# Performance work log

Measured on AMD Instinct MI355X. Metric: run time of the kernel, lower is better.

## Reference

```python
import jax, jax.numpy as jnp
import numpy as np

HEADS = 8
DIM_HEAD = 64
BOTTLENECK = 40


def setup_inputs() -> dict:
    key = jax.random.key(0)
    ks = jax.random.split(key, 10)
    b, n, qs = 4, 1024, 256
    inner = HEADS * DIM_HEAD
    s = lambda fan_in: 1.0 / np.sqrt(fan_in)
    return {
        "x":   jax.random.normal(ks[0], (b, n, qs), dtype=jnp.float32),
        # weights stored as (in, out) so forward is x @ W
        "wq1": jax.random.normal(ks[1], (qs, BOTTLENECK), dtype=jnp.float32) * s(qs),
        "wq2": jax.random.normal(ks[2], (BOTTLENECK, inner), dtype=jnp.float32) * s(BOTTLENECK),
        "wk1": jax.random.normal(ks[3], (qs, BOTTLENECK), dtype=jnp.float32) * s(qs),
        "wk2": jax.random.normal(ks[4], (BOTTLENECK, inner), dtype=jnp.float32) * s(BOTTLENECK),
        "wv1": jax.random.normal(ks[5], (qs, BOTTLENECK), dtype=jnp.float32) * s(qs),
        "wv2": jax.random.normal(ks[6], (BOTTLENECK, inner), dtype=jnp.float32) * s(BOTTLENECK),
        "wo":  jax.random.normal(ks[7], (inner, qs), dtype=jnp.float32) * s(inner),
        "bo":  jax.random.normal(ks[8], (qs,), dtype=jnp.float32) * 0.01,
    }


def reference(x, wq1, wq2, wk1, wk2, wv1, wv2, wo, bo):
    b, n, _ = x.shape
    h, d = HEADS, DIM_HEAD
    scale = d ** -0.5

    # bottlenecked QKV projections (40-dim), SiLU on K bottleneck
    q = (x @ wq1) @ wq2                       # (b, n, h*d)
    k = jax.nn.silu(x @ wk1) @ wk2            # (b, n, h*d)
    v = (x @ wv1) @ wv2                       # (b, n, h*d)

    def split(t):  # 'b n (h d) -> b (h n) d'
        return t.reshape(b, n, h, d).transpose(0, 2, 1, 3).reshape(b, h * n, d)

    q, k, v = split(q), split(k), split(v)

    sim = jnp.einsum('bid,bjd->bij', q, k) * scale   # (b, h*n, h*n)
    attn = jax.nn.softmax(sim, axis=-1)
    out = jnp.einsum('bij,bjd->bid', attn, v)        # (b, h*n, d)

    # 'b (h n) d -> b n (h d)'
    out = out.reshape(b, h, n, d).transpose(0, 2, 1, 3).reshape(b, n, h * d)
    return out @ wo + bo
```

## Files before the change

### kernel.cpp

```cpp
#include <hip/hip_runtime.h>
#include <hip/hip_bf16.h>


#define B_    4
#define H_    8
#define NSEQ  1024
#define SEQ   8192
#define DH    64
#define QS    256
#define INNER 512
#define QSCALE 0.18033688011112042f

#define KVSW_BATCH 524288

typedef __bf16 bf16x8 __attribute__((ext_vector_type(8)));
typedef float floatx4 __attribute__((ext_vector_type(4)));

__global__ __launch_bounds__(1024) void qkv_kernel(
    const float* __restrict__ x,
    const float* __restrict__ wq1, const float* __restrict__ wq2,
    const float* __restrict__ wk1, const float* __restrict__ wk2,
    const float* __restrict__ wv1, const float* __restrict__ wv2,
    __hip_bfloat16* __restrict__ Qg, __hip_bfloat16* __restrict__ KSg,
    __hip_bfloat16* __restrict__ VSg)
{
  const int tid  = threadIdx.x;
  const int b    = blockIdx.x >> 6;
  const int nblk = blockIdx.x & 63;
  const int n0   = nblk << 4;

  __shared__ __align__(16) float xs[16][260];
  __shared__ __align__(16) float tb2[2][3][16][40];
  __shared__ __align__(16) float tb[3][16][40];
  __shared__ __align__(16) __hip_bfloat16 qb[16][520];
  __shared__ __align__(16) __hip_bfloat16 kb[16][520];
  __shared__ __align__(16) __hip_bfloat16 vb[512][20];

  for (int i = tid; i < 16 * 256; i += 1024) {
    const int r = i >> 8, c = i & 255;
    xs[r][c] = x[((size_t)b * NSEQ + n0 + r) * QS + c];
  }
  __syncthreads();

  if (tid < 960) {
    const int ks  = (tid >= 480) ? 1 : 0;
    const int t2  = tid - ks * 480;
    const int p   = t2 / 160;
    const int rem = t2 - p * 160;
    const int r   = rem / 10;
    const int bn  = (rem - r * 10) * 4;
    const float* w1 = (p == 0) ? wq1 : (p == 1) ? wk1 : wv1;
    float a0 = 0.f, a1 = 0.f, a2 = 0.f, a3 = 0.f;
    #pragma unroll 4
    for (int c4 = ks * 32; c4 < ks * 32 + 32; ++c4) {
      const float4 xv = *(const float4*)(&xs[r][c4 * 4]);
      const float4 wa = *(const float4*)(w1 + (c4 * 4 + 0) * 40 + bn);
      const float4 wb = *(const float4*)(w1 + (c4 * 4 + 1) * 40 + bn);
      const float4 wc = *(const float4*)(w1 + (c4 * 4 + 2) * 40 + bn);
      const float4 wd = *(const float4*)(w1 + (c4 * 4 + 3) * 40 + bn);
      a0 += xv.x * wa.x + xv.y * wb.x + xv.z * wc.x + xv.w * wd.x;
      a1 += xv.x * wa.y + xv.y * wb.y + xv.z * wc.y + xv.w * wd.y;
      a2 += xv.x * wa.z + xv.y * wb.z + xv.z * wc.z + xv.w * wd.z;
      a3 += xv.x * wa.w + xv.y * wb.w + xv.z * wc.w + xv.w * wd.w;
    }
    tb2[ks][p][r][bn + 0] = a0; tb2[ks][p][r][bn + 1] = a1;
    tb2[ks][p][r][bn + 2] = a2; tb2[ks][p][r][bn + 3] = a3;
  }
  __syncthreads();

  if (tid < 480) {
    const int p   = tid / 160;
    const int rem = tid - p * 160;
    const int r   = rem / 10;
    const int bn  = (rem - r * 10) * 4;
    const float4 h0 = *(const float4*)(&tb2[0][p][r][bn]);
    const float4 h1 = *(const float4*)(&tb2[1][p][r][bn]);
    float a0 = h0.x + h1.x, a1 = h0.y + h1.y, a2 = h0.z + h1.z, a3 = h0.w + h1.w;
    if (p == 1) {
      a0 = a0 / (1.f + __expf(-a0));
      a1 = a1 / (1.f + __expf(-a1));
      a2 = a2 / (1.f + __expf(-a2));
      a3 = a3 / (1.f + __expf(-a3));
    }
    tb[p][r][bn + 0] = a0; tb[p][r][bn + 1] = a1;
    tb[p][r][bn + 2] = a2; tb[p][r][bn + 3] = a3;
  }
  __syncthreads();

  #pragma unroll
  for (int pass = 0; pass < 3; ++pass) {
    const int p  = pass;
    const int cq = tid & 127;
    const int rq = (tid >> 7) & 7;
    const int c  = cq * 4, r0 = rq * 2;
    const float* w2 = (p == 0) ? wq2 : (p == 1) ? wk2 : wv2;
    const float scale = (p == 0) ? QSCALE : 1.0f;
    float acc[2][4];
    #pragma unroll
    for (int i = 0; i < 2; ++i)
      #pragma unroll
      for (int j = 0; j < 4; ++j) acc[i][j] = 0.f;

    #pragma unroll 2
    for (int jb = 0; jb < 10; ++jb) {
      const float4 w0 = *(const float4*)(w2 + (jb * 4 + 0) * INNER + c);
      const float4 w1r = *(const float4*)(w2 + (jb * 4 + 1) * INNER + c);
      const float4 w2r = *(const float4*)(w2 + (jb * 4 + 2) * INNER + c);
      const float4 w3 = *(const float4*)(w2 + (jb * 4 + 3) * INNER + c);
      #pragma unroll
      for (int ri = 0; ri < 2; ++ri) {
        const float4 tv = *(const float4*)(&tb[p][r0 + ri][jb * 4]);
        acc[ri][0] += tv.x * w0.x + tv.y * w1r.x + tv.z * w2r.x + tv.w * w3.x;
        acc[ri][1] += tv.x * w0.y + tv.y * w1r.y + tv.z * w2r.y + tv.w * w3.y;
        acc[ri][2] += tv.x * w0.z + tv.y * w1r.z + tv.z * w2r.z + tv.w * w3.z;
        acc[ri][3] += tv.x * w0.w + tv.y * w1r.w + tv.z * w2r.w + tv.w * w3.w;
      }
    }
    #pragma unroll
    for (int ri = 0; ri < 2; ++ri)
      #pragma unroll
      for (int ci = 0; ci < 4; ++ci) {
        const int cc = c + ci;
        const float v = acc[ri][ci] * scale;
        if (p == 0)      qb[r0 + ri][cc] = __float2bfloat16(v);
        else if (p == 1) kb[r0 + ri][cc] = __float2bfloat16(v);
        else             vb[cc][r0 + ri] = __float2bfloat16(v);
      }
  }
  __syncthreads();

  {
    const int i  = tid;
    const int h  = i >> 7;
    const int r  = (i >> 3) & 15;
    const int d8 = i & 7;
    *(float4*)(Qg + ((size_t)b * SEQ + h * NSEQ + n0 + r) * DH + d8 * 8) =
        *(const float4*)(&qb[r][h * 64 + d8 * 8]);
  }

  {
    const int i    = tid;
    const int h    = i >> 7;
    const int ks   = (i >> 6) & 1;
    const int quad = (i >> 4) & 3;
    const int r    = i & 15;
    const int lane = quad * 16 + r;
    const size_t dst = (size_t)b * KVSW_BATCH
        + ((size_t)((h * 64 + nblk) * 2 + ks) * 64 + lane) * 8;
    *(float4*)(KSg + dst) = *(const float4*)(&kb[r][h * 64 + ks * 32 + quad * 8]);
  }

  {
    const int st  = nblk & 1;
    const int p32 = nblk >> 1;
    #pragma unroll
    for (int pass = 0; pass < 2; ++pass) {
      const int i   = tid + pass * 1024;
      const int h   = i >> 8;
      const int dnt = (i >> 6) & 3;
      const int dm  = (i >> 2) & 15;
      const int rg  = i & 3;
      const int lane = rg * 16 + dm;
      const size_t dst = (size_t)b * KVSW_BATCH
          + ((size_t)((h * 32 + p32) * 4 + dnt) * 64 + lane) * 8 + st * 4;
      *(uint2*)(VSg + dst) = *(const uint2*)(&vb[h * 64 + dnt * 16 + dm][rg * 4]);
    }
  }
}

struct PairBuf {
  bf16x8 k[2][2];
  bf16x8 v[4];
};

__global__ __launch_bounds__(256, 3) void attn_kernel(
    const __hip_bfloat16* __restrict__ Qg,
    const __hip_bfloat16* __restrict__ KSg,
    const __hip_bfloat16* __restrict__ VSg,
    float* __restrict__ OPg,
    float* __restrict__ PSg)
{
  __shared__ float Osh[4][16][68];
  __shared__ float psums[4][64];

  const int tid  = threadIdx.x;
  const int wave = tid >> 6;
  const int lane = tid & 63;
  const int lrow = lane & 15;
  const int quad = lane >> 4;

  const int xcd   = blockIdx.x & 7;
  const int idx   = blockIdx.x >> 3;
  const int b     = xcd >> 1;
  const int half  = idx & 1;
  const int qtile = (xcd & 1) * 64 + (idx >> 1);
  const int qbase = qtile * 64;

  const __hip_bfloat16* Qb  = Qg + ((size_t)b * SEQ + qbase) * DH;
  const __hip_bfloat16* kp0 = KSg + (size_t)b * KVSW_BATCH + half * 262144
                              + (size_t)wave * 65536 + lane * 8;
  const __hip_bfloat16* vp0 = VSg + (size_t)b * KVSW_BATCH + half * 262144
                              + (size_t)wave * 65536 + lane * 8;

  bf16x8 qf[4][2];
  #pragma unroll
  for (int mt = 0; mt < 4; ++mt)
    #pragma unroll
    for (int s = 0; s < 2; ++s)
      qf[mt][s] = *(const bf16x8*)(Qb + (mt * 16 + lrow) * DH + s * 32 + quad * 8);

  floatx4 oacc[4][4];
  #pragma unroll
  for (int mt = 0; mt < 4; ++mt)
    #pragma unroll
    for (int dnt = 0; dnt < 4; ++dnt)
      oacc[mt][dnt] = (floatx4){0.f, 0.f, 0.f, 0.f};
  float psum[4] = {0.f, 0.f, 0.f, 0.f};

  #pragma unroll 2
  for (int pair = 0; pair < 32; ++pair) {
    PairBuf pb;
    const __hip_bfloat16* kp = kp0 + pair * 2048;
    pb.k[0][0] = *(const bf16x8*)(kp);
    pb.k[0][1] = *(const bf16x8*)(kp + 512);
    pb.k[1][0] = *(const bf16x8*)(kp + 1024);
    pb.k[1][1] = *(const bf16x8*)(kp + 1536);
    const __hip_bfloat16* vp = vp0 + pair * 2048;
    #pragma unroll
    for (int dnt = 0; dnt < 4; ++dnt)
      pb.v[dnt] = *(const bf16x8*)(vp + dnt * 512);

    #pragma unroll
    for (int mt = 0; mt < 4; ++mt) {
      floatx4 s0 = (floatx4){0.f, 0.f, 0.f, 0.f};
      floatx4 s1 = (floatx4){0.f, 0.f, 0.f, 0.f};
      s0 = __builtin_amdgcn_mfma_f32_16x16x32_bf16(pb.k[0][0], qf[mt][0], s0, 0, 0, 0);
      s0 = __builtin_amdgcn_mfma_f32_16x16x32_bf16(pb.k[0][1], qf[mt][1], s0, 0, 0, 0);
      s1 = __builtin_amdgcn_mfma_f32_16x16x32_bf16(pb.k[1][0], qf[mt][0], s1, 0, 0, 0);
      s1 = __builtin_amdgcn_mfma_f32_16x16x32_bf16(pb.k[1][1], qf[mt][1], s1, 0, 0, 0);
      float p[8];
      #pragma unroll
      for (int r = 0; r < 4; ++r) {
        p[r]     = __builtin_amdgcn_exp2f(s0[r]);
        p[4 + r] = __builtin_amdgcn_exp2f(s1[r]);
      }
      psum[mt] += ((p[0] + p[1]) + (p[2] + p[3])) + ((p[4] + p[5]) + (p[6] + p[7]));
      bf16x8 pa;
      #pragma unroll
      for (int j = 0; j < 8; ++j) pa[j] = (__bf16)p[j];
      #pragma unroll
      for (int dnt = 0; dnt < 4; ++dnt)
        oacc[mt][dnt] = __builtin_amdgcn_mfma_f32_16x16x32_bf16(pa, pb.v[dnt], oacc[mt][dnt], 0, 0, 0);
    }
  }

  #pragma unroll
  for (int mt = 0; mt < 4; ++mt) {
    float s = psum[mt];
    s += __shfl_xor(s, 16, 64);
    s += __shfl_xor(s, 32, 64);
    psum[mt] = s;
  }
  if (quad == 0) {
    #pragma unroll
    for (int mt = 0; mt < 4; ++mt)
      psums[wave][mt * 16 + lrow] = psum[mt];
  }

  const size_t opbase = ((size_t)half * B_ + b) * SEQ + qbase;

  #pragma unroll
  for (int mt = 0; mt < 4; ++mt) {
    #pragma unroll
    for (int dnt = 0; dnt < 4; ++dnt)
      #pragma unroll
      for (int r = 0; r < 4; ++r)
        Osh[wave][quad * 4 + r][dnt * 16 + lrow] = oacc[mt][dnt][r];
    __syncthreads();

    {
      const int q16 = tid >> 4;
      const int d0  = (tid & 15) * 4;
      float4 a0 = *(const float4*)(&Osh[0][q16][d0]);
      float4 a1 = *(const float4*)(&Osh[1][q16][d0]);
      float4 a2 = *(const float4*)(&Osh[2][q16][d0]);
      float4 a3 = *(const float4*)(&Osh[3][q16][d0]);
      float4 res;
      res.x = (a0.x + a1.x) + (a2.x + a3.x);
      res.y = (a0.y + a1.y) + (a2.y + a3.y);
      res.z = (a0.z + a1.z) + (a2.z + a3.z);
      res.w = (a0.w + a1.w) + (a2.w + a3.w);
      *(float4*)(OPg + (opbase + mt * 16 + q16) * DH + d0) = res;
    }
    if (mt == 0 && tid < 64) {
      const float tot = (psums[0][tid] + psums[1][tid]) + (psums[2][tid] + psums[3][tid]);
      PSg[opbase + tid] = tot;
    }
    __syncthreads();
  }
}

__global__ __launch_bounds__(512) void out_kernel(
    const float* __restrict__ OPg, const float* __restrict__ PSg,
    const float* __restrict__ wo, const float* __restrict__ bo,
    float* __restrict__ out)
{
  const int tid = threadIdx.x;
  const int b   = blockIdx.x >> 6;
  const int n0  = (blockIdx.x & 63) << 4;

  __shared__ __align__(16) float os[16][520];
  __shared__ __align__(16) float wot[2][16][260];
  __shared__ float invs[16][8];

  if (tid < 128) {
    const int r = tid >> 3, h = tid & 7;
    const size_t row = (size_t)b * SEQ + h * NSEQ + n0 + r;
    invs[r][h] = 1.0f / (PSg[row] + PSg[(size_t)B_ * SEQ + row]);
  }
  __syncthreads();

  for (int i = tid; i < 2048; i += 512) {
    const int r  = i >> 7;
    const int c4 = (i & 127) * 4;
    const int h  = c4 >> 6;
    const size_t idx = ((size_t)b * SEQ + h * NSEQ + n0 + r) * DH + (c4 & 63);
    const float4 p0 = *(const float4*)(OPg + idx);
    const float4 p1 = *(const float4*)(OPg + (size_t)B_ * SEQ * DH + idx);
    const float inv = invs[r][c4 >> 6];
    float4 m;
    m.x = (p0.x + p1.x) * inv;
    m.y = (p0.y + p1.y) * inv;
    m.z = (p0.z + p1.z) * inv;
    m.w = (p0.w + p1.w) * inv;
    *(float4*)(&os[r][c4]) = m;
  }

  {
    const int c0 = tid, c1 = tid + 512;
    const float4 v0 = *(const float4*)(wo + (size_t)(c0 >> 6) * QS + (c0 & 63) * 4);
    const float4 v1 = *(const float4*)(wo + (size_t)(c1 >> 6) * QS + (c1 & 63) * 4);
    *(float4*)(&wot[0][c0 >> 6][(c0 & 63) * 4]) = v0;
    *(float4*)(&wot[0][c1 >> 6][(c1 & 63) * 4]) = v1;
  }
  __syncthreads();

  const int oq = tid & 63;
  const int rq = tid >> 6;
  const int o  = oq * 4;
  const int r0 = rq * 2;

  float acc[2][4];
  #pragma unroll
  for (int i = 0; i < 2; ++i)
    #pragma unroll
    for (int j = 0; j < 4; ++j) acc[i][j] = 0.f;

  for (int kt = 0; kt < 32; ++kt) {
    const int cur = kt & 1;
    float4 pf0, pf1;
    const int c0 = tid, c1 = tid + 512;
    if (kt < 31) {
      const int kb = (kt + 1) * 16;
      pf0 = *(const float4*)(wo + (size_t)(kb + (c0 >> 6)) * QS + (c0 & 63) * 4);
      pf1 = *(const float4*)(wo + (size_t)(kb + (c1 >> 6)) * QS + (c1 & 63) * 4);
    }

    const int kbase = kt * 16;
    #pragma unroll
    for (int kq = 0; kq < 4; ++kq) {
      const float4 ov0 = *(const float4*)(&os[r0][kbase + kq * 4]);
      const float4 ov1 = *(const float4*)(&os[r0 + 1][kbase + kq * 4]);
      #pragma unroll
      for (int j = 0; j < 4; ++j) {
        const float4 w = *(const float4*)(&wot[cur][kq * 4 + j][o]);
        const float a = (j == 0) ? ov0.x : (j == 1) ? ov0.y : (j == 2) ? ov0.z : ov0.w;
        const float bq = (j == 0) ? ov1.x : (j == 1) ? ov1.y : (j == 2) ? ov1.z : ov1.w;
        acc[0][0] += a * w.x; acc[0][1] += a * w.y;
        acc[0][2] += a * w.z; acc[0][3] += a * w.w;
        acc[1][0] += bq * w.x; acc[1][1] += bq * w.y;
        acc[1][2] += bq * w.z; acc[1][3] += bq * w.w;
      }
    }

    if (kt < 31) {
      *(float4*)(&wot[cur ^ 1][c0 >> 6][(c0 & 63) * 4]) = pf0;
      *(float4*)(&wot[cur ^ 1][c1 >> 6][(c1 & 63) * 4]) = pf1;
    }
    __syncthreads();
  }

  const float4 bv = *(const float4*)(bo + o);
  #pragma unroll
  for (int ri = 0; ri < 2; ++ri) {
    float4 res;
    res.x = acc[ri][0] + bv.x;
    res.y = acc[ri][1] + bv.y;
    res.z = acc[ri][2] + bv.z;
    res.w = acc[ri][3] + bv.w;
    *(float4*)(out + ((size_t)b * NSEQ + n0 + r0 + ri) * QS + o) = res;
  }
}

extern "C" void kernel_launch(void* const* d_in, const int* in_sizes, int n_in,
                              void* d_out, int out_size, void* d_ws, size_t ws_size,
                              hipStream_t stream) {
  const float* x   = (const float*)d_in[0];
  const float* wq1 = (const float*)d_in[1];
  const float* wq2 = (const float*)d_in[2];
  const float* wk1 = (const float*)d_in[3];
  const float* wk2 = (const float*)d_in[4];
  const float* wv1 = (const float*)d_in[5];
  const float* wv2 = (const float*)d_in[6];
  const float* wo  = (const float*)d_in[7];
  const float* bo  = (const float*)d_in[8];
  float* out = (float*)d_out;

  __hip_bfloat16* Qg  = (__hip_bfloat16*)d_ws;
  __hip_bfloat16* KSg = Qg + (size_t)B_ * SEQ * DH;
  __hip_bfloat16* VSg = KSg + (size_t)B_ * KVSW_BATCH;
  float*          OPg = (float*)(VSg + (size_t)B_ * KVSW_BATCH);
  float*          PSg = OPg + 2 * (size_t)B_ * SEQ * DH;

  qkv_kernel<<<256, 1024, 0, stream>>>(x, wq1, wq2, wk1, wk2, wv1, wv2, Qg, KSg, VSg);
  attn_kernel<<<1024, 256, 0, stream>>>(Qg, KSg, VSg, OPg, PSg);
  out_kernel<<<256, 512, 0, stream>>>(OPg, PSg, wo, bo, out);
}
```

Before: 195.3 us.

## Split QKV projection kernel across Q/K/V into separate smaller blocks

The QKV kernel now launches three times as many 512-thread blocks, each handling one of Q, K or V for a 16-row tile, instead of one 1024-thread block doing all three. The first-stage reduction is split four ways over the input dimension, and a single shared output buffer replaces the three per-projection buffers. The aim is higher occupancy and more parallelism in the small projection stage. In exchange the x tile is loaded three times and the per-block work shrinks.

```diff
diff --git a/kernel.cpp b/kernel.cpp
--- a/kernel.cpp
+++ b/kernel.cpp
@@ -16,7 +16,7 @@
 typedef __bf16 bf16x8 __attribute__((ext_vector_type(8)));
 typedef float floatx4 __attribute__((ext_vector_type(4)));
 
-__global__ __launch_bounds__(1024) void qkv_kernel(
+__global__ __launch_bounds__(512, 4) void qkv_kernel(
     const float* __restrict__ x,
     const float* __restrict__ wq1, const float* __restrict__ wq2,
     const float* __restrict__ wk1, const float* __restrict__ wk2,
@@ -25,34 +25,38 @@
     __hip_bfloat16* __restrict__ VSg)
 {
   const int tid  = threadIdx.x;
-  const int b    = blockIdx.x >> 6;
-  const int nblk = blockIdx.x & 63;
+  const int p    = blockIdx.x >> 8;
+  const int rest = blockIdx.x & 255;
+  const int b    = rest >> 6;
+  const int nblk = rest & 63;
   const int n0   = nblk << 4;
 
   __shared__ __align__(16) float xs[16][260];
-  __shared__ __align__(16) float tb2[2][3][16][40];
-  __shared__ __align__(16) float tb[3][16][40];
-  __shared__ __align__(16) __hip_bfloat16 qb[16][520];
-  __shared__ __align__(16) __hip_bfloat16 kb[16][520];
-  __shared__ __align__(16) __hip_bfloat16 vb[512][20];
-
-  for (int i = tid; i < 16 * 256; i += 1024) {
-    const int r = i >> 8, c = i & 255;
-    xs[r][c] = x[((size_t)b * NSEQ + n0 + r) * QS + c];
-  }
-  __syncthreads();
-
-  if (tid < 960) {
-    const int ks  = (tid >= 480) ? 1 : 0;
-    const int t2  = tid - ks * 480;
-    const int p   = t2 / 160;
-    const int rem = t2 - p * 160;
+  __shared__ __align__(16) float tb2[4][16][40];
+  __shared__ __align__(16) float tb[16][40];
+  __shared__ __align__(16) __hip_bfloat16 ob[10400];
+
+  const float* w1 = (p == 0) ? wq1 : (p == 1) ? wk1 : wv1;
+  const float* w2 = (p == 0) ? wq2 : (p == 1) ? wk2 : wv2;
+
+  #pragma unroll
+  for (int j = 0; j < 2; ++j) {
+    const int i  = tid + j * 512;
+    const int r  = i >> 6;
+    const int c4 = (i & 63) << 2;
+    *(float4*)(&xs[r][c4]) =
+        *(const float4*)(x + ((size_t)b * NSEQ + n0 + r) * QS + c4);
+  }
+  __syncthreads();
+
+  for (int t = tid; t < 640; t += 512) {
+    const int ks  = t / 160;
+    const int rem = t - ks * 160;
     const int r   = rem / 10;
     const int bn  = (rem - r * 10) * 4;
-    const float* w1 = (p == 0) ? wq1 : (p == 1) ? wk1 : wv1;
     float a0 = 0.f, a1 = 0.f, a2 = 0.f, a3 = 0.f;
     #pragma unroll 4
-    for (int c4 = ks * 32; c4 < ks * 32 + 32; ++c4) {
+    for (int c4 = ks * 16; c4 < ks * 16 + 16; ++c4) {
       const float4 xv = *(const float4*)(&xs[r][c4 * 4]);
       const float4 wa = *(const float4*)(w1 + (c4 * 4 + 0) * 40 + bn);
       const float4 wb = *(const float4*)(w1 + (c4 * 4 + 1) * 40 + bn);
@@ -63,53 +67,53 @@
       a2 += xv.x * wa.z + xv.y * wb.z + xv.z * wc.z + xv.w * wd.z;
       a3 += xv.x * wa.w + xv.y * wb.w + xv.z * wc.w + xv.w * wd.w;
     }
-    tb2[ks][p][r][bn + 0] = a0; tb2[ks][p][r][bn + 1] = a1;
-    tb2[ks][p][r][bn + 2] = a2; tb2[ks][p][r][bn + 3] = a3;
-  }
-  __syncthreads();
-
-  if (tid < 480) {
-    const int p   = tid / 160;
-    const int rem = tid - p * 160;
-    const int r   = rem / 10;
-    const int bn  = (rem - r * 10) * 4;
-    const float4 h0 = *(const float4*)(&tb2[0][p][r][bn]);
-    const float4 h1 = *(const float4*)(&tb2[1][p][r][bn]);
-    float a0 = h0.x + h1.x, a1 = h0.y + h1.y, a2 = h0.z + h1.z, a3 = h0.w + h1.w;
+    tb2[ks][r][bn + 0] = a0; tb2[ks][r][bn + 1] = a1;
+    tb2[ks][r][bn + 2] = a2; tb2[ks][r][bn + 3] = a3;
+  }
+  __syncthreads();
+
+  if (tid < 160) {
+    const int r  = tid / 10;
+    const int bn = (tid - r * 10) * 4;
+    const float4 h0 = *(const float4*)(&tb2[0][r][bn]);
+    const float4 h1 = *(const float4*)(&tb2[1][r][bn]);
+    const float4 h2 = *(const float4*)(&tb2[2][r][bn]);
+    const float4 h3 = *(const float4*)(&tb2[3][r][bn]);
+    float a0 = (h0.x + h1.x) + (h2.x + h3.x);
+    float a1 = (h0.y + h1.y) + (h2.y + h3.y);
+    float a2 = (h0.z + h1.z) + (h2.z + h3.z);
+    float a3 = (h0.w + h1.w) + (h2.w + h3.w);
     if (p == 1) {
       a0 = a0 / (1.f + __expf(-a0));
       a1 = a1 / (1.f + __expf(-a1));
       a2 = a2 / (1.f + __expf(-a2));
       a3 = a3 / (1.f + __expf(-a3));
     }
-    tb[p][r][bn + 0] = a0; tb[p][r][bn + 1] = a1;
-    tb[p][r][bn + 2] = a2; tb[p][r][bn + 3] = a3;
-  }
-  __syncthreads();
-
-  #pragma unroll
-  for (int pass = 0; pass < 3; ++pass) {
-    const int p  = pass;
+    tb[r][bn + 0] = a0; tb[r][bn + 1] = a1;
+    tb[r][bn + 2] = a2; tb[r][bn + 3] = a3;
+  }
+  __syncthreads();
+
+  {
     const int cq = tid & 127;
-    const int rq = (tid >> 7) & 7;
-    const int c  = cq * 4, r0 = rq * 2;
-    const float* w2 = (p == 0) ? wq2 : (p == 1) ? wk2 : wv2;
+    const int rq = tid >> 7;
+    const int c  = cq * 4, r0 = rq * 4;
     const float scale = (p == 0) ? QSCALE : 1.0f;
-    float acc[2][4];
-    #pragma unroll
-    for (int i = 0; i < 2; ++i)
+    float acc[4][4];
+    #pragma unroll
+    for (int i = 0; i < 4; ++i)
       #pragma unroll
       for (int j = 0; j < 4; ++j) acc[i][j] = 0.f;
 
     #pragma unroll 2
     for (int jb = 0; jb < 10; ++jb) {
-      const float4 w0 = *(const float4*)(w2 + (jb * 4 + 0) * INNER + c);
+      const float4 w0  = *(const float4*)(w2 + (jb * 4 + 0) * INNER + c);
       const float4 w1r = *(const float4*)(w2 + (jb * 4 + 1) * INNER + c);
       const float4 w2r = *(const float4*)(w2 + (jb * 4 + 2) * INNER + c);
-      const float4 w3 = *(const float4*)(w2 + (jb * 4 + 3) * INNER + c);
-      #pragma unroll
-      for (int ri = 0; ri < 2; ++ri) {
-        const float4 tv = *(const float4*)(&tb[p][r0 + ri][jb * 4]);
+      const float4 w3  = *(const float4*)(w2 + (jb * 4 + 3) * INNER + c);
+      #pragma unroll
+      for (int ri = 0; ri < 4; ++ri) {
+        const float4 tv = *(const float4*)(&tb[r0 + ri][jb * 4]);
         acc[ri][0] += tv.x * w0.x + tv.y * w1r.x + tv.z * w2r.x + tv.w * w3.x;
         acc[ri][1] += tv.x * w0.y + tv.y * w1r.y + tv.z * w2r.y + tv.w * w3.y;
         acc[ri][2] += tv.x * w0.z + tv.y * w1r.z + tv.z * w2r.z + tv.w * w3.z;
@@ -117,45 +121,46 @@
       }
     }
     #pragma unroll
-    for (int ri = 0; ri < 2; ++ri)
+    for (int ri = 0; ri < 4; ++ri)
       #pragma unroll
       for (int ci = 0; ci < 4; ++ci) {
         const int cc = c + ci;
         const float v = acc[ri][ci] * scale;
-        if (p == 0)      qb[r0 + ri][cc] = __float2bfloat16(v);
-        else if (p == 1) kb[r0 + ri][cc] = __float2bfloat16(v);
-        else             vb[cc][r0 + ri] = __float2bfloat16(v);
+        if (p == 2) ob[cc * 20 + r0 + ri]    = __float2bfloat16(v);
+        else        ob[(r0 + ri) * 520 + cc] = __float2bfloat16(v);
       }
   }
   __syncthreads();
 
-  {
-    const int i  = tid;
-    const int h  = i >> 7;
-    const int r  = (i >> 3) & 15;
-    const int d8 = i & 7;
-    *(float4*)(Qg + ((size_t)b * SEQ + h * NSEQ + n0 + r) * DH + d8 * 8) =
-        *(const float4*)(&qb[r][h * 64 + d8 * 8]);
-  }
-
-  {
-    const int i    = tid;
-    const int h    = i >> 7;
-    const int ks   = (i >> 6) & 1;
-    const int quad = (i >> 4) & 3;
-    const int r    = i & 15;
-    const int lane = quad * 16 + r;
-    const size_t dst = (size_t)b * KVSW_BATCH
-        + ((size_t)((h * 64 + nblk) * 2 + ks) * 64 + lane) * 8;
-    *(float4*)(KSg + dst) = *(const float4*)(&kb[r][h * 64 + ks * 32 + quad * 8]);
-  }
-
-  {
+  if (p == 0) {
+    #pragma unroll
+    for (int j = 0; j < 2; ++j) {
+      const int i  = tid + j * 512;
+      const int h  = i >> 7;
+      const int r  = (i >> 3) & 15;
+      const int d8 = i & 7;
+      *(float4*)(Qg + ((size_t)b * SEQ + h * NSEQ + n0 + r) * DH + d8 * 8) =
+          *(const float4*)(&ob[r * 520 + h * 64 + d8 * 8]);
+    }
+  } else if (p == 1) {
+    #pragma unroll
+    for (int j = 0; j < 2; ++j) {
+      const int i    = tid + j * 512;
+      const int h    = i >> 7;
+      const int ks2  = (i >> 6) & 1;
+      const int quad = (i >> 4) & 3;
+      const int r    = i & 15;
+      const int lane = quad * 16 + r;
+      const size_t dst = (size_t)b * KVSW_BATCH
+          + ((size_t)((h * 64 + nblk) * 2 + ks2) * 64 + lane) * 8;
+      *(float4*)(KSg + dst) = *(const float4*)(&ob[r * 520 + h * 64 + ks2 * 32 + quad * 8]);
+    }
+  } else {
     const int st  = nblk & 1;
     const int p32 = nblk >> 1;
     #pragma unroll
-    for (int pass = 0; pass < 2; ++pass) {
-      const int i   = tid + pass * 1024;
+    for (int pass = 0; pass < 4; ++pass) {
+      const int i   = tid + pass * 512;
       const int h   = i >> 8;
       const int dnt = (i >> 6) & 3;
       const int dm  = (i >> 2) & 15;
@@ -163,7 +168,7 @@
       const int lane = rg * 16 + dm;
       const size_t dst = (size_t)b * KVSW_BATCH
           + ((size_t)((h * 32 + p32) * 4 + dnt) * 64 + lane) * 8 + st * 4;
-      *(uint2*)(VSg + dst) = *(const uint2*)(&vb[h * 64 + dnt * 16 + dm][rg * 4]);
+      *(uint2*)(VSg + dst) = *(const uint2*)(&ob[(h * 64 + dnt * 16 + dm) * 20 + rg * 4]);
     }
   }
 }
@@ -422,7 +427,7 @@
   float*          OPg = (float*)(VSg + (size_t)B_ * KVSW_BATCH);
   float*          PSg = OPg + 2 * (size_t)B_ * SEQ * DH;
 
-  qkv_kernel<<<256, 1024, 0, stream>>>(x, wq1, wq2, wk1, wk2, wv1, wv2, Qg, KSg, VSg);
+  qkv_kernel<<<768, 512, 0, stream>>>(x, wq1, wq2, wk1, wk2, wv1, wv2, Qg, KSg, VSg);
   attn_kernel<<<1024, 256, 0, stream>>>(Qg, KSg, VSg, OPg, PSg);
   out_kernel<<<256, 512, 0, stream>>>(OPg, PSg, wo, bo, out);
 }
```

New measurement: 191.9 us. No clear change (-1.7%).
